# Kernel tuning notes

Measured on AMD Instinct MI355X. Metric: run time of the kernel, lower is better.

## Reference

```python
import jax, jax.numpy as jnp
import numpy as np

N = 2048          # target nodes
N_NODES = 2048    # neighbor pool
D_IN = 256
D_EDGE = 16
D_HID = 32
D_OUT = 256


def _mlp(h, w1, b1, w2, b2):
    # Linear -> Tanh -> Linear
    return jnp.tanh(h @ w1 + b1) @ w2 + b2


def setup_inputs() -> dict:
    key = jax.random.key(0)
    ks = jax.random.split(key, 20)
    s = 0.05
    inp = {
        "x": jax.random.normal(ks[0], (N, D_IN), jnp.float32),
        "neibs": jax.random.normal(ks[1], (N_NODES, D_IN), jnp.float32),
        "edge_emb": jax.random.normal(ks[2], (N * N_NODES, D_EDGE), jnp.float32),
        # multiplicative binary mask (float, as in original ws * mask)
        "mask": (jax.random.uniform(ks[3], (N, N_NODES)) < 0.7).astype(jnp.float32),
        "ax_w1": jax.random.normal(ks[4], (D_IN, D_HID), jnp.float32) * s,
        "ax_b1": jnp.zeros((D_HID,), jnp.float32),
        "ax_w2": jax.random.normal(ks[5], (D_HID, D_HID), jnp.float32) * s,
        "ax_b2": jnp.zeros((D_HID,), jnp.float32),
        "an_w1": jax.random.normal(ks[6], (D_IN, D_HID), jnp.float32) * s,
        "an_b1": jnp.zeros((D_HID,), jnp.float32),
        "an_w2": jax.random.normal(ks[7], (D_HID, D_HID), jnp.float32) * s,
        "an_b2": jnp.zeros((D_HID,), jnp.float32),
        "ae_w1": jax.random.normal(ks[8], (D_EDGE, D_HID), jnp.float32) * s,
        "ae_b1": jnp.zeros((D_HID,), jnp.float32),
        "ae_w2": jax.random.normal(ks[9], (D_HID, D_HID), jnp.float32) * s,
        "ae_b2": jnp.zeros((D_HID,), jnp.float32),
        "fcx_w": jax.random.normal(ks[10], (2 * D_IN, D_OUT), jnp.float32) * s,
        "fcx_b": jnp.zeros((D_OUT,), jnp.float32),
    }
    return inp


def reference(x, neibs, edge_emb, mask,
              ax_w1, ax_b1, ax_w2, ax_b2,
              an_w1, an_b1, an_w2, an_b2,
              ae_w1, ae_b1, ae_w2, ae_b2,
              fcx_w, fcx_b):
    x_att = _mlp(x, ax_w1, ax_b1, ax_w2, ax_b2)          # (N, H)
    neib_att = _mlp(neibs, an_w1, an_b1, an_w2, an_b2)   # (n_nodes, H)
    # edge attention is computed in the original forward but never used (dead code)
    _edge_att = _mlp(edge_emb, ae_w1, ae_b1, ae_w2, ae_b2)
    # multiplicative masking (NOT additive -inf), then softmax over neighbors
    ws = jnp.einsum('nh,mh->nm', x_att, neib_att) * mask  # (N, n_nodes)
    ws = jax.nn.softmax(ws, axis=1)
    agg_neib = jax.nn.sigmoid(ws @ neibs)                 # (N, D_IN)
    # concat_node=False path: concat -> fc_x -> sigmoid; dropout is identity (eval)
    out = jax.nn.sigmoid(jnp.concatenate([x, agg_neib], axis=1) @ fcx_w + fcx_b)
    return out
```

## Files before the change

### kernel.cpp

```cpp
#include <hip/hip_runtime.h>
#include <hip/hip_bf16.h>
#include <math.h>

#define NROWS 2048
#define DIN 256
#define DH 32
#define DOUT 256

typedef unsigned short ushort_t;
typedef unsigned int uint_t;
typedef __attribute__((ext_vector_type(8))) short short8;
typedef __attribute__((ext_vector_type(4))) float floatx4;
typedef __attribute__((ext_vector_type(4))) ushort_t ushortx4;

__device__ __forceinline__ float bf2f(uint_t u) {
    union { uint_t i; float f; } v; v.i = u << 16; return v.f;
}
__device__ __forceinline__ ushort_t f2bf(float f) {
    __hip_bfloat16 h = __float2bfloat16(f);
    union { __hip_bfloat16 h; ushort_t u; } v; v.h = h; return v.u;
}
__device__ __forceinline__ float sigm(float v) { return 1.0f / (1.0f + __expf(-v)); }

#define PSTR 2056
#define ASTR 520

__global__ __launch_bounds__(256) void prep_kernel(
    const float* __restrict__ x, const float* __restrict__ neibs,
    const float* __restrict__ ax_w1, const float* __restrict__ ax_b1,
    const float* __restrict__ ax_w2, const float* __restrict__ ax_b2,
    const float* __restrict__ an_w1, const float* __restrict__ an_b1,
    const float* __restrict__ an_w2, const float* __restrict__ an_b2,
    const float* __restrict__ fcx_w,
    ushort_t* __restrict__ x_attB, short8* __restrict__ n_attP,
    short8* __restrict__ B_pack, short8* __restrict__ W_pack)
{
    __shared__ float smem[32 * 256];
    const int t = threadIdx.x;
    const int b = blockIdx.x;

    if (b < 512) {
        float (*srow)[DIN] = (float (*)[DIN])smem;
        float* hbuf = smem + 8 * DIN;
        float* sbuf = smem + 8 * DIN + 8 * DH;

        const bool is_x = b < 256;
        const int row0 = (is_x ? b : b - 256) * 8;
        const float* __restrict__ in = is_x ? x : neibs;
        const float* __restrict__ w1 = is_x ? ax_w1 : an_w1;
        const float* __restrict__ b1 = is_x ? ax_b1 : an_b1;
        const float* __restrict__ w2 = is_x ? ax_w2 : an_w2;
        const float* __restrict__ b2 = is_x ? ax_b2 : an_b2;

        const int r = t >> 5, c = t & 31;
        {
            const float4* in4 = (const float4*)(in + (size_t)(row0 + r) * DIN);
            float4 a = in4[c * 2], bb = in4[c * 2 + 1];
            *(float4*)&srow[r][c * 8] = a;
            *(float4*)&srow[r][c * 8 + 4] = bb;
        }
        __syncthreads();

        float s = b1[c];
#pragma unroll 8
        for (int k = 0; k < DIN; ++k) s += srow[r][k] * w1[k * DH + c];
        s = tanhf(s);
        hbuf[r * DH + c] = s;
        __syncthreads();

        float s2 = b2[c];
#pragma unroll
        for (int j = 0; j < DH; ++j) s2 += hbuf[r * DH + j] * w2[j * DH + c];

        if (is_x) {
            x_attB[(size_t)(row0 + r) * DH + c] = f2bf(s2);
        } else {
            sbuf[r * DH + c] = s2;
            __syncthreads();
            if (t < 32) {
                const int r2 = t >> 2, q = t & 3;
                const int row = row0 + r2;
                short8 v;
#pragma unroll
                for (int j = 0; j < 8; ++j) v[j] = (short)f2bf(sbuf[r2 * DH + q * 8 + j]);
                n_attP[(row >> 4) * 64 + q * 16 + (row & 15)] = v;
            }
        }
    } else if (b < 576) {
        const int s = b - 512;
        float* tile = smem;
#pragma unroll
        for (int i = 0; i < 8; ++i) {
            const int e = i * 256 + t;
            const int row = e >> 6, c4 = e & 63;
            const float4 v = ((const float4*)neibs)[(size_t)(32 * s + row) * 64 + c4];
            *(float4*)&tile[row * 256 + c4 * 4] = v;
        }
        __syncthreads();
#pragma unroll
        for (int i = 0; i < 4; ++i) {
            const int G = i * 256 + t;
            const int n = G & 15, q = (G >> 4) & 3, ct = G >> 6;
            const int col = ct * 16 + n;
            short8 v;
#pragma unroll
            for (int j = 0; j < 8; ++j) v[j] = (short)f2bf(tile[(8 * q + j) * 256 + col]);
            B_pack[s * 1024 + G] = v;
        }
    } else {
        const int s = b - 576;
        float* tile = smem;
#pragma unroll
        for (int i = 0; i < 8; ++i) {
            const int e = i * 256 + t;
            const int row = e >> 6, c4 = e & 63;
            const float4 v = ((const float4*)fcx_w)[(size_t)(32 * s + row) * 64 + c4];
            *(float4*)&tile[row * 256 + c4 * 4] = v;
        }
        __syncthreads();
#pragma unroll
        for (int i = 0; i < 4; ++i) {
            const int G = i * 256 + t;
            const int n = G & 15, q = (G >> 4) & 3, ct = G >> 6;
            const int col = ct * 16 + n;
            short8 v;
#pragma unroll
            for (int j = 0; j < 8; ++j) v[j] = (short)f2bf(tile[(8 * q + j) * 256 + col]);
            W_pack[s * 1024 + G] = v;
        }
    }
}

__global__ __launch_bounds__(512, 2) void attn_kernel(
    const float* __restrict__ x, const float* __restrict__ mask,
    const ushort_t* __restrict__ x_attB, const short8* __restrict__ n_attP,
    const short8* __restrict__ B_pack, const short8* __restrict__ W_pack,
    const float* __restrict__ fcx_b, float* __restrict__ out)
{
    __shared__ __align__(16) ushort_t pTr[8 * PSTR];
    __shared__ __align__(16) ushort_t ATr[8 * ASTR];
    __shared__ float row_inv[8];

    const int t = threadIdx.x;
    const int n0 = blockIdx.x * 8;
    const int w = t >> 6, lane = t & 63;
    const int q = lane >> 4, nn = lane & 15;
    const int arow = lane & 7;
    const int gl = lane >> 4;
    const int prow0 = (gl & 1) * 4 + (gl >> 1) * 2;
    const int reg0 = (gl >> 1) * 2;

    {
        const int r = t >> 6, c4 = t & 63;
        const float4 v = *(const float4*)(x + (size_t)(n0 + r) * DIN + c4 * 4);
        ushortx4 o;
        o.x = f2bf(v.x); o.y = f2bf(v.y); o.z = f2bf(v.z); o.w = f2bf(v.w);
        *(ushortx4*)&ATr[r * ASTR + c4 * 4] = o;
    }

    const short8 av_s = *(const short8*)(x_attB + (size_t)(n0 + arow) * DH + q * 8);
#pragma unroll 4
    for (int i = 0; i < 16; ++i) {
        const int tl = w * 16 + i;
        const short8 bv = n_attP[tl * 64 + lane];
        floatx4 c = __builtin_amdgcn_mfma_f32_16x16x32_bf16(
            av_s, bv, (floatx4){0.f, 0.f, 0.f, 0.f}, 0, 0, 0);
        const int m = tl * 16 + nn;
#pragma unroll
        for (int u = 0; u < 2; ++u) {
            const int row = prow0 + u;
            const float sv = c[reg0 + u] * mask[(size_t)(n0 + row) * NROWS + m];
            pTr[row * PSTR + m] = f2bf(sv);
        }
    }
    __syncthreads();

    {
        ushort_t* prow = pTr + w * PSTR;
        uint_t raw[16];
        float mx = -1e30f;
#pragma unroll
        for (int j = 0; j < 16; ++j) {
            raw[j] = *(const uint_t*)(prow + j * 128 + 2 * lane);
            mx = fmaxf(mx, fmaxf(bf2f(raw[j] & 0xffffu), bf2f(raw[j] >> 16)));
        }
#pragma unroll
        for (int off = 32; off >= 1; off >>= 1) mx = fmaxf(mx, __shfl_xor(mx, off));
        float sum = 0.f;
#pragma unroll
        for (int j = 0; j < 16; ++j) {
            const float e0 = __expf(bf2f(raw[j] & 0xffffu) - mx);
            const float e1 = __expf(bf2f(raw[j] >> 16) - mx);
            sum += e0 + e1;
            *(uint_t*)(prow + j * 128 + 2 * lane) =
                (uint_t)f2bf(e0) | ((uint_t)f2bf(e1) << 16);
        }
#pragma unroll
        for (int off = 32; off >= 1; off >>= 1) sum += __shfl_xor(sum, off);
        if (lane == 0) row_inv[w] = 1.f / sum;
    }
    __syncthreads();

    const char* aBase = (const char*)pTr + arow * (PSTR * 2);
    floatx4 accP[2][2];
#pragma unroll
    for (int tt = 0; tt < 2; ++tt)
#pragma unroll
        for (int pr = 0; pr < 2; ++pr) accP[tt][pr] = (floatx4){0.f, 0.f, 0.f, 0.f};

#pragma unroll 4
    for (int s = 0; s < 64; ++s) {
        const short8 av = *(const short8*)(aBase + s * 64 + q * 16);
        const int pr = s & 1;
#pragma unroll
        for (int tt = 0; tt < 2; ++tt) {
            const short8 bv = B_pack[(s * 16 + 2 * w + tt) * 64 + lane];
            accP[tt][pr] = __builtin_amdgcn_mfma_f32_16x16x32_bf16(av, bv, accP[tt][pr], 0, 0, 0);
        }
    }
#pragma unroll
    for (int tt = 0; tt < 2; ++tt) {
        const floatx4 a = accP[tt][0] + accP[tt][1];
        const int n = w * 32 + tt * 16 + nn;
#pragma unroll
        for (int u = 0; u < 2; ++u) {
            const int row = prow0 + u;
            ATr[row * ASTR + 256 + n] = f2bf(sigm(a[reg0 + u] * row_inv[row]));
        }
    }
    __syncthreads();

    const char* a2 = (const char*)ATr + arow * (ASTR * 2);
    floatx4 acc2[2][2];
#pragma unroll
    for (int tt = 0; tt < 2; ++tt)
#pragma unroll
        for (int pr = 0; pr < 2; ++pr) acc2[tt][pr] = (floatx4){0.f, 0.f, 0.f, 0.f};

#pragma unroll
    for (int s = 0; s < 16; ++s) {
        const short8 av = *(const short8*)(a2 + s * 64 + q * 16);
        const int pr = s & 1;
#pragma unroll
        for (int tt = 0; tt < 2; ++tt) {
            const short8 bv = W_pack[(s * 16 + 2 * w + tt) * 64 + lane];
            acc2[tt][pr] = __builtin_amdgcn_mfma_f32_16x16x32_bf16(av, bv, acc2[tt][pr], 0, 0, 0);
        }
    }
#pragma unroll
    for (int tt = 0; tt < 2; ++tt) {
        const floatx4 a = acc2[tt][0] + acc2[tt][1];
        const int n = w * 32 + tt * 16 + nn;
        const float bias = fcx_b[n];
#pragma unroll
        for (int u = 0; u < 2; ++u) {
            const int row = prow0 + u;
            out[(size_t)(n0 + row) * DOUT + n] = sigm(a[reg0 + u] + bias);
        }
    }
}

extern "C" void kernel_launch(void* const* d_in, const int* in_sizes, int n_in,
                              void* d_out, int out_size, void* d_ws, size_t ws_size,
                              hipStream_t stream) {
    const float* x      = (const float*)d_in[0];
    const float* neibs  = (const float*)d_in[1];
    const float* mask   = (const float*)d_in[3];
    const float* ax_w1  = (const float*)d_in[4];
    const float* ax_b1  = (const float*)d_in[5];
    const float* ax_w2  = (const float*)d_in[6];
    const float* ax_b2  = (const float*)d_in[7];
    const float* an_w1  = (const float*)d_in[8];
    const float* an_b1  = (const float*)d_in[9];
    const float* an_w2  = (const float*)d_in[10];
    const float* an_b2  = (const float*)d_in[11];
    const float* fcx_w  = (const float*)d_in[16];
    const float* fcx_b  = (const float*)d_in[17];
    float* out = (float*)d_out;

    char* ws = (char*)d_ws;
    ushort_t* x_attB = (ushort_t*)ws;
    short8*   n_attP = (short8*)(ws + 131072);
    short8*   B_pack = (short8*)(ws + 262144);
    short8*   W_pack = (short8*)(ws + 1310720);

    prep_kernel<<<592, 256, 0, stream>>>(
        x, neibs, ax_w1, ax_b1, ax_w2, ax_b2,
        an_w1, an_b1, an_w2, an_b2, fcx_w,
        x_attB, n_attP, B_pack, W_pack);

    attn_kernel<<<256, 512, 0, stream>>>(
        x, mask, x_attB, n_attP, B_pack, W_pack, fcx_b, out);
}
```

Baseline: 373.6 us.

## Process 16 target rows per block to fill MFMA M dimension

Each attention block now handles 16 target rows instead of 8, so every 16x16 MFMA tile uses all its rows instead of half. The B_pack and W_pack operand loads are spread over twice as many rows, cutting global and L2 traffic per output row and halving the MFMA count for the aggregation GEMMs. In exchange, LDS use per block doubles and the grid shrinks to 128 blocks, which leaves many of the 256 CUs idle and may lower occupancy.

Result: no change. 376.4 us (+0.8%).

```diff
diff --git a/kernel.cpp b/kernel.cpp
--- a/kernel.cpp
+++ b/kernel.cpp
@@ -137,21 +137,21 @@
     const short8* __restrict__ B_pack, const short8* __restrict__ W_pack,
     const float* __restrict__ fcx_b, float* __restrict__ out)
 {
-    __shared__ __align__(16) ushort_t pTr[8 * PSTR];
-    __shared__ __align__(16) ushort_t ATr[8 * ASTR];
-    __shared__ float row_inv[8];
+    __shared__ __align__(16) ushort_t pTr[16 * PSTR];
+    __shared__ __align__(16) ushort_t ATr[16 * ASTR];
+    __shared__ float row_inv[16];
 
     const int t = threadIdx.x;
-    const int n0 = blockIdx.x * 8;
+    const int n0 = blockIdx.x * 16;
     const int w = t >> 6, lane = t & 63;
     const int q = lane >> 4, nn = lane & 15;
-    const int arow = lane & 7;
-    const int gl = lane >> 4;
-    const int prow0 = (gl & 1) * 4 + (gl >> 1) * 2;
-    const int reg0 = (gl >> 1) * 2;
-
-    {
-        const int r = t >> 6, c4 = t & 63;
+    const int arow = lane & 15;
+    const int crow0 = (lane >> 4) * 4;
+
+#pragma unroll
+    for (int i = 0; i < 2; ++i) {
+        const int e = i * 512 + t;
+        const int r = e >> 6, c4 = e & 63;
         const float4 v = *(const float4*)(x + (size_t)(n0 + r) * DIN + c4 * 4);
         ushortx4 o;
         o.x = f2bf(v.x); o.y = f2bf(v.y); o.z = f2bf(v.z); o.w = f2bf(v.w);
@@ -167,16 +167,18 @@
             av_s, bv, (floatx4){0.f, 0.f, 0.f, 0.f}, 0, 0, 0);
         const int m = tl * 16 + nn;
 #pragma unroll
-        for (int u = 0; u < 2; ++u) {
-            const int row = prow0 + u;
-            const float sv = c[reg0 + u] * mask[(size_t)(n0 + row) * NROWS + m];
+        for (int rg = 0; rg < 4; ++rg) {
+            const int row = crow0 + rg;
+            const float sv = c[rg] * mask[(size_t)(n0 + row) * NROWS + m];
             pTr[row * PSTR + m] = f2bf(sv);
         }
     }
     __syncthreads();
 
-    {
-        ushort_t* prow = pTr + w * PSTR;
+#pragma unroll
+    for (int rr = 0; rr < 2; ++rr) {
+        const int row = 2 * w + rr;
+        ushort_t* prow = pTr + row * PSTR;
         uint_t raw[16];
         float mx = -1e30f;
 #pragma unroll
@@ -197,7 +199,7 @@
         }
 #pragma unroll
         for (int off = 32; off >= 1; off >>= 1) sum += __shfl_xor(sum, off);
-        if (lane == 0) row_inv[w] = 1.f / sum;
+        if (lane == 0) row_inv[row] = 1.f / sum;
     }
     __syncthreads();
 
@@ -223,9 +225,9 @@
         const floatx4 a = accP[tt][0] + accP[tt][1];
         const int n = w * 32 + tt * 16 + nn;
 #pragma unroll
-        for (int u = 0; u < 2; ++u) {
-            const int row = prow0 + u;
-            ATr[row * ASTR + 256 + n] = f2bf(sigm(a[reg0 + u] * row_inv[row]));
+        for (int rg = 0; rg < 4; ++rg) {
+            const int row = crow0 + rg;
+            ATr[row * ASTR + 256 + n] = f2bf(sigm(a[rg] * row_inv[row]));
         }
     }
     __syncthreads();
@@ -253,9 +255,9 @@
         const int n = w * 32 + tt * 16 + nn;
         const float bias = fcx_b[n];
 #pragma unroll
-        for (int u = 0; u < 2; ++u) {
-            const int row = prow0 + u;
-            out[(size_t)(n0 + row) * DOUT + n] = sigm(a[reg0 + u] + bias);
+        for (int rg = 0; rg < 4; ++rg) {
+            const int row = crow0 + rg;
+            out[(size_t)(n0 + row) * DOUT + n] = sigm(a[rg] + bias);
         }
     }
 }
@@ -289,6 +291,6 @@
         an_w1, an_b1, an_w2, an_b2, fcx_w,
         x_attB, n_attP, B_pack, W_pack);
 
-    attn_kernel<<<256, 512, 0, stream>>>(
+    attn_kernel<<<128, 512, 0, stream>>>(
         x, mask, x_attB, n_attP, B_pack, W_pack, fcx_b, out);
 }
```
